# Kernel tuning notes

Measured on AMD Instinct MI355X. Metric: run time of the kernel, lower is better.

Reference implementation:

```python
import jax, jax.numpy as jnp
import numpy as np

H = 256  # hidden size

def setup_inputs() -> dict:
    key = jax.random.key(0)
    k1, k2, k3 = jax.random.split(key, 3)
    B, T, D = 64, 2048, 256
    x = jax.random.normal(k1, (B, T, D), dtype=jnp.float32)
    Wx = jax.random.normal(k2, (D, 4 * H), dtype=jnp.float32) * (1.0 / np.sqrt(D))
    Wh = jax.random.normal(k3, (H, 4 * H), dtype=jnp.float32) * (1.0 / np.sqrt(H))
    bx = jnp.zeros((4 * H,), dtype=jnp.float32)
    bh = jnp.zeros((4 * H,), dtype=jnp.float32)
    return {"x": x, "Wx": Wx, "Wh": Wh, "bx": bx, "bh": bh}

def reference(x, Wx, Wh, bx, bh):
    B, T, D = x.shape
    # Precompute input projections for all timesteps: [T, B, 4H]
    xg = jnp.einsum('btd,dg->tbg', x, Wx) + bx

    def step(carry, xg_t):
        h_prev, c_prev = carry
        gates = xg_t + h_prev @ Wh + bh          # [B, 4H]
        f, i, o, chat = jnp.split(gates, 4, axis=-1)
        f_t = jax.nn.sigmoid(f)
        i_t = jax.nn.sigmoid(i)
        o_t = jax.nn.sigmoid(o)
        c_t = f_t * c_prev + i_t * jnp.tanh(chat)
        h_t = o_t * jnp.tanh(c_t)
        return (h_t, c_t), h_t

    h0 = jnp.zeros((B, H), dtype=x.dtype)
    c0 = jnp.zeros((B, H), dtype=x.dtype)
    (h_T, c_T), hs = jax.lax.scan(step, (h0, c0), xg)  # hs: [T, B, H]
    outputs = jnp.transpose(hs, (1, 0, 2))  # batch_first: [B, T, H]
    return outputs, (h_T, c_T)
```

## Files before the change

### kernel.cpp

```cpp
#include <hip/hip_runtime.h>
#include <stdint.h>

#define H 256
#define BB 64
#define TT 2048
#define G4 1024
#define LDX 264

typedef __attribute__((ext_vector_type(8))) short short8;
typedef __attribute__((ext_vector_type(4))) float float4_;
typedef unsigned long long ull;
typedef unsigned short ushort_t;

static __device__ __forceinline__ float bfhi2f(ushort_t u) {
    union { unsigned int i; float f; } v; v.i = ((unsigned int)u) << 16; return v.f;
}
static __device__ __forceinline__ ushort_t f2bf(float x) {
    union { float f; unsigned int i; } v; v.f = x;
    unsigned int u = v.i;
    return (ushort_t)((u + 0x7FFFu + ((u >> 16) & 1u)) >> 16);
}
static __device__ __forceinline__ void split2(float x, ushort_t& hi, ushort_t& lo) {
    hi = f2bf(x);
    lo = f2bf(x - bfhi2f(hi));
}
static __device__ __forceinline__ float sigm(float x) { return 1.0f / (1.0f + __expf(-x)); }
static __device__ __forceinline__ float tanh_(float x) { return 2.0f / (1.0f + __expf(-2.0f * x)) - 1.0f; }

__global__ __launch_bounds__(256) void split_w(const float* __restrict__ Wx,
                                               const float* __restrict__ Wh,
                                               ushort_t* __restrict__ planes) {
    const int g = blockIdx.x & 1023;
    const int mat = blockIdx.x >> 10;
    const int k = threadIdx.x;
    const float* src = mat ? Wh : Wx;
    float v = src[(size_t)k * G4 + g];
    ushort_t hi, lo; split2(v, hi, lo);
    ushort_t* ph = planes + (size_t)mat * 2 * G4 * 256;
    ph[g * 256 + k] = hi;
    ph[(size_t)G4 * 256 + g * 256 + k] = lo;
}

__global__ __launch_bounds__(256, 1) void lstm_scan(
        const float* __restrict__ x,
        const float* __restrict__ bx,
        const float* __restrict__ bh,
        const ushort_t* __restrict__ WxTh, const ushort_t* __restrict__ WxTl,
        const ushort_t* __restrict__ WhTh, const ushort_t* __restrict__ WhTl,
        float* __restrict__ out0,
        float* __restrict__ outh,
        float* __restrict__ outc,
        ull* __restrict__ hbuf,
        unsigned int* __restrict__ cnt) {
    __shared__ ushort_t xah[16 * LDX], xal[16 * LDX];
    __shared__ ushort_t hsh[16 * LDX], hsl[16 * LDX];
    __shared__ float gatesL[1024];
    __shared__ float cst[256];
    __shared__ float bL[64];

    const int tid = threadIdx.x;
    const int grp = blockIdx.x & 3;
    const int s = blockIdx.x >> 2;
    const int lane = tid & 63, wave = tid >> 6;
    const int lm = lane & 15, lq = lane >> 4;
    const int pb = tid >> 4, pj = tid & 15;

    if (tid < 64) {
        int g = ((tid >> 4) << 8) + (s << 4) + (tid & 15);
        bL[tid] = bx[g] + bh[g];
    }
    cst[tid] = 0.0f;

    const size_t wrow = ((size_t)((wave << 8) + (s << 4) + lm)) * 256;
    short8 fxh[8], fxl[8], fhh[8], fhl[8];
#pragma unroll
    for (int kc = 0; kc < 8; ++kc) {
        fxh[kc] = *(const short8*)(WxTh + wrow + kc * 32 + lq * 8);
        fxl[kc] = *(const short8*)(WxTl + wrow + kc * 32 + lq * 8);
        fhh[kc] = *(const short8*)(WhTh + wrow + kc * 32 + lq * 8);
        fhl[kc] = *(const short8*)(WhTl + wrow + kc * 32 + lq * 8);
    }

    const float* xp0 = x + ((size_t)(grp * 16 + pb)) * TT * 256 + pj * 16;
    float* o0 = out0 + ((size_t)(grp * 16 + pb)) * TT * H + (s << 4) + pj;

    for (int t = 0; t < TT; ++t) {
        const float* xp = xp0 + (size_t)t * 256;
        float4_ v0 = *(const float4_*)(xp);
        float4_ v1 = *(const float4_*)(xp + 4);
        float4_ v2 = *(const float4_*)(xp + 8);
        float4_ v3 = *(const float4_*)(xp + 12);
        const int rb = pb * LDX + pj * 16;
#pragma unroll
        for (int q = 0; q < 4; ++q) {
            float4_ vv = (q == 0) ? v0 : (q == 1) ? v1 : (q == 2) ? v2 : v3;
            union { ushort_t u[4]; ull q8; } ph_, pl_;
#pragma unroll
            for (int e = 0; e < 4; ++e) {
                ushort_t hi, lo; split2(vv[e], hi, lo);
                ph_.u[e] = hi; pl_.u[e] = lo;
            }
            *(ull*)(xah + rb + q * 4) = ph_.q8;
            *(ull*)(xal + rb + q * 4) = pl_.q8;
        }
        __syncthreads();

        float4_ acc = {};
#pragma unroll
        for (int kc = 0; kc < 8; ++kc) {
            short8 ah = *(const short8*)(xah + lm * LDX + kc * 32 + lq * 8);
            short8 al = *(const short8*)(xal + lm * LDX + kc * 32 + lq * 8);
            acc = __builtin_amdgcn_mfma_f32_16x16x32_bf16(ah, fxh[kc], acc, 0, 0, 0);
            acc = __builtin_amdgcn_mfma_f32_16x16x32_bf16(ah, fxl[kc], acc, 0, 0, 0);
            acc = __builtin_amdgcn_mfma_f32_16x16x32_bf16(al, fxh[kc], acc, 0, 0, 0);
        }

        if (tid == 0 && t > 0) {
            unsigned int target = 16u * (unsigned int)t;
            while (__hip_atomic_load(&cnt[grp], __ATOMIC_ACQUIRE, __HIP_MEMORY_SCOPE_AGENT) < target)
                __builtin_amdgcn_s_sleep(1);
        }
        __syncthreads();

        const int par = t & 1;
        const ull* hpH = hbuf + ((size_t)(par * 4 + grp)) * 2048;
        const ull* hpL = hpH + 1024;
        {
            const int u0 = tid * 4;
            const int hb = u0 >> 6;
            const int ho = (u0 & 63) * 4;
            ull a0 = __hip_atomic_load(hpH + u0 + 0, __ATOMIC_RELAXED, __HIP_MEMORY_SCOPE_AGENT);
            ull a1 = __hip_atomic_load(hpH + u0 + 1, __ATOMIC_RELAXED, __HIP_MEMORY_SCOPE_AGENT);
            ull a2 = __hip_atomic_load(hpH + u0 + 2, __ATOMIC_RELAXED, __HIP_MEMORY_SCOPE_AGENT);
            ull a3 = __hip_atomic_load(hpH + u0 + 3, __ATOMIC_RELAXED, __HIP_MEMORY_SCOPE_AGENT);
            ull b0 = __hip_atomic_load(hpL + u0 + 0, __ATOMIC_RELAXED, __HIP_MEMORY_SCOPE_AGENT);
            ull b1 = __hip_atomic_load(hpL + u0 + 1, __ATOMIC_RELAXED, __HIP_MEMORY_SCOPE_AGENT);
            ull b2 = __hip_atomic_load(hpL + u0 + 2, __ATOMIC_RELAXED, __HIP_MEMORY_SCOPE_AGENT);
            ull b3 = __hip_atomic_load(hpL + u0 + 3, __ATOMIC_RELAXED, __HIP_MEMORY_SCOPE_AGENT);
            *(ull*)(hsh + hb * LDX + ho + 0)  = a0;
            *(ull*)(hsh + hb * LDX + ho + 4)  = a1;
            *(ull*)(hsh + hb * LDX + ho + 8)  = a2;
            *(ull*)(hsh + hb * LDX + ho + 12) = a3;
            *(ull*)(hsl + hb * LDX + ho + 0)  = b0;
            *(ull*)(hsl + hb * LDX + ho + 4)  = b1;
            *(ull*)(hsl + hb * LDX + ho + 8)  = b2;
            *(ull*)(hsl + hb * LDX + ho + 12) = b3;
        }
        __syncthreads();

#pragma unroll
        for (int kc = 0; kc < 8; ++kc) {
            short8 ah = *(const short8*)(hsh + lm * LDX + kc * 32 + lq * 8);
            short8 al = *(const short8*)(hsl + lm * LDX + kc * 32 + lq * 8);
            acc = __builtin_amdgcn_mfma_f32_16x16x32_bf16(ah, fhh[kc], acc, 0, 0, 0);
            acc = __builtin_amdgcn_mfma_f32_16x16x32_bf16(ah, fhl[kc], acc, 0, 0, 0);
            acc = __builtin_amdgcn_mfma_f32_16x16x32_bf16(al, fhh[kc], acc, 0, 0, 0);
        }
#pragma unroll
        for (int r = 0; r < 4; ++r)
            gatesL[(wave << 8) + ((lq * 4 + r) << 4) + lm] = acc[r];
        __syncthreads();

        float g0 = gatesL[tid]       + bL[pj];
        float g1 = gatesL[256 + tid] + bL[16 + pj];
        float g2 = gatesL[512 + tid] + bL[32 + pj];
        float g3 = gatesL[768 + tid] + bL[48 + pj];
        float ft = sigm(g0), it = sigm(g1), ot = sigm(g2), ch = tanh_(g3);
        float c = ft * cst[tid] + it * ch;
        cst[tid] = c;
        float hv = ot * tanh_(c);
        o0[(size_t)t * H] = hv;
        ushort_t hhi, hlo; split2(hv, hhi, hlo);
        ushort_t* pnH = (ushort_t*)(hbuf + ((size_t)(((par ^ 1) * 4) + grp)) * 2048);
        ushort_t* pnL = pnH + 4096;
        const int e = (pb << 8) + (s << 4) + pj;
        __hip_atomic_store(pnH + e, hhi, __ATOMIC_RELAXED, __HIP_MEMORY_SCOPE_AGENT);
        __hip_atomic_store(pnL + e, hlo, __ATOMIC_RELAXED, __HIP_MEMORY_SCOPE_AGENT);
        if (t == TT - 1) {
            outh[(grp * 16 + pb) * H + (s << 4) + pj] = hv;
            outc[(grp * 16 + pb) * H + (s << 4) + pj] = c;
        }
        __syncthreads();
        if (tid == 0)
            __hip_atomic_fetch_add(&cnt[grp], 1u, __ATOMIC_RELEASE, __HIP_MEMORY_SCOPE_AGENT);
    }
}

extern "C" void kernel_launch(void* const* d_in, const int* in_sizes, int n_in,
                              void* d_out, int out_size, void* d_ws, size_t ws_size,
                              hipStream_t stream) {
    (void)in_sizes; (void)n_in; (void)out_size; (void)ws_size;
    const float* x  = (const float*)d_in[0];
    const float* Wx = (const float*)d_in[1];
    const float* Wh = (const float*)d_in[2];
    const float* bx = (const float*)d_in[3];
    const float* bh = (const float*)d_in[4];
    float* out0 = (float*)d_out;
    float* outh = out0 + (size_t)BB * TT * H;
    float* outc = outh + (size_t)BB * H;

    ull* hbuf = (ull*)d_ws;
    unsigned int* cnt = (unsigned int*)((char*)d_ws + 131072);
    ushort_t* planes = (ushort_t*)((char*)d_ws + 131072 + 128);

    hipMemsetAsync(d_ws, 0, 131072 + 128, stream);
    split_w<<<2048, 256, 0, stream>>>(Wx, Wh, planes);
    lstm_scan<<<64, 256, 0, stream>>>(x, bx, bh,
        planes,
        planes + (size_t)G4 * 256,
        planes + (size_t)2 * G4 * 256,
        planes + (size_t)3 * G4 * 256,
        out0, outh, outc, hbuf, cnt);
}
```

Baseline: 8.485 ms.

## Replace counter barrier with tagged h exchange and prefetch next x

Drops the per-group atomic counter and its trailing block barrier. Each h value is now stored as fp32 with a 7-bit timestep tag packed into its low mantissa bits, so consumers spin-poll the data itself until every tag matches. The x load for the next step is prefetched into registers and overlaps the current step. This also removes the bf16 hi/lo split on the writer side. The cost is that h (and the outputs) lose 7 mantissa bits, and every thread polls global memory rather than a single thread.

```diff
diff --git a/kernel.cpp b/kernel.cpp
--- a/kernel.cpp
+++ b/kernel.cpp
@@ -11,6 +11,7 @@
 typedef __attribute__((ext_vector_type(4))) float float4_;
 typedef unsigned long long ull;
 typedef unsigned short ushort_t;
+typedef unsigned int uint_t;
 
 static __device__ __forceinline__ float bfhi2f(ushort_t u) {
     union { unsigned int i; float f; } v; v.i = ((unsigned int)u) << 16; return v.f;
@@ -50,8 +51,7 @@
         float* __restrict__ out0,
         float* __restrict__ outh,
         float* __restrict__ outc,
-        ull* __restrict__ hbuf,
-        unsigned int* __restrict__ cnt) {
+        uint_t* __restrict__ hbuf) {
     __shared__ ushort_t xah[16 * LDX], xal[16 * LDX];
     __shared__ ushort_t hsh[16 * LDX], hsl[16 * LDX];
     __shared__ float gatesL[1024];
@@ -84,26 +84,33 @@
     const float* xp0 = x + ((size_t)(grp * 16 + pb)) * TT * 256 + pj * 16;
     float* o0 = out0 + ((size_t)(grp * 16 + pb)) * TT * H + (s << 4) + pj;
 
+    float4_ xv[4];
+#pragma unroll
+    for (int q = 0; q < 4; ++q) xv[q] = *(const float4_*)(xp0 + q * 4);
+
+    const int rb = pb * LDX + pj * 16;
+
     for (int t = 0; t < TT; ++t) {
-        const float* xp = xp0 + (size_t)t * 256;
-        float4_ v0 = *(const float4_*)(xp);
-        float4_ v1 = *(const float4_*)(xp + 4);
-        float4_ v2 = *(const float4_*)(xp + 8);
-        float4_ v3 = *(const float4_*)(xp + 12);
-        const int rb = pb * LDX + pj * 16;
 #pragma unroll
         for (int q = 0; q < 4; ++q) {
-            float4_ vv = (q == 0) ? v0 : (q == 1) ? v1 : (q == 2) ? v2 : v3;
             union { ushort_t u[4]; ull q8; } ph_, pl_;
 #pragma unroll
             for (int e = 0; e < 4; ++e) {
-                ushort_t hi, lo; split2(vv[e], hi, lo);
+                ushort_t hi, lo; split2(xv[q][e], hi, lo);
                 ph_.u[e] = hi; pl_.u[e] = lo;
             }
             *(ull*)(xah + rb + q * 4) = ph_.q8;
             *(ull*)(xal + rb + q * 4) = pl_.q8;
         }
         __syncthreads();
+
+        const uint_t* hp = hbuf + ((((t & 1) << 2) + grp) << 12) + (pb << 8) + (pj << 4);
+        uint_t w[16];
+        if (t > 0) {
+#pragma unroll
+            for (int e = 0; e < 16; ++e)
+                w[e] = __hip_atomic_load(hp + e, __ATOMIC_RELAXED, __HIP_MEMORY_SCOPE_AGENT);
+        }
 
         float4_ acc = {};
 #pragma unroll
@@ -115,47 +122,47 @@
             acc = __builtin_amdgcn_mfma_f32_16x16x32_bf16(al, fxh[kc], acc, 0, 0, 0);
         }
 
-        if (tid == 0 && t > 0) {
-            unsigned int target = 16u * (unsigned int)t;
-            while (__hip_atomic_load(&cnt[grp], __ATOMIC_ACQUIRE, __HIP_MEMORY_SCOPE_AGENT) < target)
-                __builtin_amdgcn_s_sleep(1);
-        }
-        __syncthreads();
-
-        const int par = t & 1;
-        const ull* hpH = hbuf + ((size_t)(par * 4 + grp)) * 2048;
-        const ull* hpL = hpH + 1024;
-        {
-            const int u0 = tid * 4;
-            const int hb = u0 >> 6;
-            const int ho = (u0 & 63) * 4;
-            ull a0 = __hip_atomic_load(hpH + u0 + 0, __ATOMIC_RELAXED, __HIP_MEMORY_SCOPE_AGENT);
-            ull a1 = __hip_atomic_load(hpH + u0 + 1, __ATOMIC_RELAXED, __HIP_MEMORY_SCOPE_AGENT);
-            ull a2 = __hip_atomic_load(hpH + u0 + 2, __ATOMIC_RELAXED, __HIP_MEMORY_SCOPE_AGENT);
-            ull a3 = __hip_atomic_load(hpH + u0 + 3, __ATOMIC_RELAXED, __HIP_MEMORY_SCOPE_AGENT);
-            ull b0 = __hip_atomic_load(hpL + u0 + 0, __ATOMIC_RELAXED, __HIP_MEMORY_SCOPE_AGENT);
-            ull b1 = __hip_atomic_load(hpL + u0 + 1, __ATOMIC_RELAXED, __HIP_MEMORY_SCOPE_AGENT);
-            ull b2 = __hip_atomic_load(hpL + u0 + 2, __ATOMIC_RELAXED, __HIP_MEMORY_SCOPE_AGENT);
-            ull b3 = __hip_atomic_load(hpL + u0 + 3, __ATOMIC_RELAXED, __HIP_MEMORY_SCOPE_AGENT);
-            *(ull*)(hsh + hb * LDX + ho + 0)  = a0;
-            *(ull*)(hsh + hb * LDX + ho + 4)  = a1;
-            *(ull*)(hsh + hb * LDX + ho + 8)  = a2;
-            *(ull*)(hsh + hb * LDX + ho + 12) = a3;
-            *(ull*)(hsl + hb * LDX + ho + 0)  = b0;
-            *(ull*)(hsl + hb * LDX + ho + 4)  = b1;
-            *(ull*)(hsl + hb * LDX + ho + 8)  = b2;
-            *(ull*)(hsl + hb * LDX + ho + 12) = b3;
-        }
-        __syncthreads();
-
-#pragma unroll
-        for (int kc = 0; kc < 8; ++kc) {
-            short8 ah = *(const short8*)(hsh + lm * LDX + kc * 32 + lq * 8);
-            short8 al = *(const short8*)(hsl + lm * LDX + kc * 32 + lq * 8);
-            acc = __builtin_amdgcn_mfma_f32_16x16x32_bf16(ah, fhh[kc], acc, 0, 0, 0);
-            acc = __builtin_amdgcn_mfma_f32_16x16x32_bf16(ah, fhl[kc], acc, 0, 0, 0);
-            acc = __builtin_amdgcn_mfma_f32_16x16x32_bf16(al, fhh[kc], acc, 0, 0, 0);
-        }
+        if (t + 1 < TT) {
+            const float* xp = xp0 + (size_t)(t + 1) * 256;
+#pragma unroll
+            for (int q = 0; q < 4; ++q) xv[q] = *(const float4_*)(xp + q * 4);
+        }
+
+        if (t > 0) {
+            const uint_t texp = (uint_t)(t & 127);
+            while (true) {
+                bool ok = true;
+#pragma unroll
+                for (int e = 0; e < 16; ++e) ok &= ((w[e] & 127u) == texp);
+                if (ok) break;
+#pragma unroll
+                for (int e = 0; e < 16; ++e)
+                    w[e] = __hip_atomic_load(hp + e, __ATOMIC_RELAXED, __HIP_MEMORY_SCOPE_AGENT);
+            }
+#pragma unroll
+            for (int q = 0; q < 4; ++q) {
+                union { ushort_t u[4]; ull q8; } ph_, pl_;
+#pragma unroll
+                for (int e = 0; e < 4; ++e) {
+                    float v = __uint_as_float(w[q * 4 + e] & ~127u);
+                    ushort_t hi, lo; split2(v, hi, lo);
+                    ph_.u[e] = hi; pl_.u[e] = lo;
+                }
+                *(ull*)(hsh + rb + q * 4) = ph_.q8;
+                *(ull*)(hsl + rb + q * 4) = pl_.q8;
+            }
+            __syncthreads();
+
+#pragma unroll
+            for (int kc = 0; kc < 8; ++kc) {
+                short8 ah = *(const short8*)(hsh + lm * LDX + kc * 32 + lq * 8);
+                short8 al = *(const short8*)(hsl + lm * LDX + kc * 32 + lq * 8);
+                acc = __builtin_amdgcn_mfma_f32_16x16x32_bf16(ah, fhh[kc], acc, 0, 0, 0);
+                acc = __builtin_amdgcn_mfma_f32_16x16x32_bf16(ah, fhl[kc], acc, 0, 0, 0);
+                acc = __builtin_amdgcn_mfma_f32_16x16x32_bf16(al, fhh[kc], acc, 0, 0, 0);
+            }
+        }
+
 #pragma unroll
         for (int r = 0; r < 4; ++r)
             gatesL[(wave << 8) + ((lq * 4 + r) << 4) + lm] = acc[r];
@@ -169,20 +176,18 @@
         float c = ft * cst[tid] + it * ch;
         cst[tid] = c;
         float hv = ot * tanh_(c);
-        o0[(size_t)t * H] = hv;
-        ushort_t hhi, hlo; split2(hv, hhi, hlo);
-        ushort_t* pnH = (ushort_t*)(hbuf + ((size_t)(((par ^ 1) * 4) + grp)) * 2048);
-        ushort_t* pnL = pnH + 4096;
-        const int e = (pb << 8) + (s << 4) + pj;
-        __hip_atomic_store(pnH + e, hhi, __ATOMIC_RELAXED, __HIP_MEMORY_SCOPE_AGENT);
-        __hip_atomic_store(pnL + e, hlo, __ATOMIC_RELAXED, __HIP_MEMORY_SCOPE_AGENT);
+
+        uint_t um = __float_as_uint(hv) & ~127u;
+        float hm = __uint_as_float(um);
+        o0[(size_t)t * H] = hm;
+
+        uint_t* hw = hbuf + (((((t & 1) ^ 1) << 2) + grp) << 12) + (pb << 8) + (s << 4) + pj;
+        __hip_atomic_store(hw, um | (uint_t)((t + 1) & 127), __ATOMIC_RELAXED, __HIP_MEMORY_SCOPE_AGENT);
+
         if (t == TT - 1) {
-            outh[(grp * 16 + pb) * H + (s << 4) + pj] = hv;
+            outh[(grp * 16 + pb) * H + (s << 4) + pj] = hm;
             outc[(grp * 16 + pb) * H + (s << 4) + pj] = c;
         }
-        __syncthreads();
-        if (tid == 0)
-            __hip_atomic_fetch_add(&cnt[grp], 1u, __ATOMIC_RELEASE, __HIP_MEMORY_SCOPE_AGENT);
     }
 }
 
@@ -199,8 +204,7 @@
     float* outh = out0 + (size_t)BB * TT * H;
     float* outc = outh + (size_t)BB * H;
 
-    ull* hbuf = (ull*)d_ws;
-    unsigned int* cnt = (unsigned int*)((char*)d_ws + 131072);
+    uint_t* hbuf = (uint_t*)d_ws;
     ushort_t* planes = (ushort_t*)((char*)d_ws + 131072 + 128);
 
     hipMemsetAsync(d_ws, 0, 131072 + 128, stream);
@@ -210,5 +214,5 @@
         planes + (size_t)G4 * 256,
         planes + (size_t)2 * G4 * 256,
         planes + (size_t)3 * G4 * 256,
-        out0, outh, outc, hbuf, cnt);
-}
+        out0, outh, outc, hbuf);
+}
```

Result: no change. 8.482 ms (-0.0%).
